# Optimization experiments

Measured on AMD Instinct MI355X. Metric: run time of the kernel, lower is better.

## Reference

```python
import jax, jax.numpy as jnp
import numpy as np

WS = 8   # window size
NH = 8   # num heads


def layernorm(x, g, b, eps=1e-5):
    m = jnp.mean(x, axis=-1, keepdims=True)
    v = jnp.var(x, axis=-1, keepdims=True)
    return (x - m) * jax.lax.rsqrt(v + eps) * g + b


def setup_inputs() -> dict:
    key = jax.random.key(0)
    ks = jax.random.split(key, 8)
    B, C, H, W = 16, 256, 64, 64
    s = 0.02
    inp = {
        "x": jax.random.normal(ks[0], (B, C, H, W), jnp.float32),
        "norm1_g": jnp.ones((C,), jnp.float32),
        "norm1_b": jnp.zeros((C,), jnp.float32),
        "qkv_w": jax.random.normal(ks[1], (3 * C, C), jnp.float32) * s,
        "qkv_b": jnp.zeros((3 * C,), jnp.float32),
        "rel_bias_table": jax.random.normal(ks[2], ((2 * WS - 1) ** 2, NH), jnp.float32) * s,
        "proj_w": jax.random.normal(ks[3], (C, C), jnp.float32) * s,
        "proj_b": jnp.zeros((C,), jnp.float32),
        "norm2_g": jnp.ones((C,), jnp.float32),
        "norm2_b": jnp.zeros((C,), jnp.float32),
        "fc1_w": jax.random.normal(ks[4], (4 * C, C), jnp.float32) * s,
        "fc1_b": jnp.zeros((4 * C,), jnp.float32),
        "fc2_w": jax.random.normal(ks[5], (C, 4 * C), jnp.float32) * s,
        "fc2_b": jnp.zeros((C,), jnp.float32),
    }
    # relative position index (Swin standard), shape (WS*WS, WS*WS), int constant
    coords = np.stack(np.meshgrid(np.arange(WS), np.arange(WS), indexing="ij")).reshape(2, -1)
    rel = (coords[:, :, None] - coords[:, None, :]).transpose(1, 2, 0)
    rel[:, :, 0] += WS - 1
    rel[:, :, 1] += WS - 1
    rel[:, :, 0] *= 2 * WS - 1
    inp["rel_index"] = jnp.asarray(rel.sum(-1), jnp.int32)
    return inp


def reference(x, norm1_g, norm1_b, qkv_w, qkv_b, rel_bias_table, proj_w, proj_b,
              norm2_g, norm2_b, fc1_w, fc1_b, fc2_w, fc2_b, rel_index):
    B, C, H, W = x.shape
    N = WS * WS
    hd = C // NH
    scale = hd ** -0.5

    xs = jnp.transpose(x, (0, 2, 3, 1)).reshape(B, H * W, C)  # b (h w) c
    shortcut = xs

    y = layernorm(xs, norm1_g, norm1_b).reshape(B, H, W, C)
    # window partition -> (B*nW, N, C); shift_size = 0 (default), no cyclic shift / mask
    y = y.reshape(B, H // WS, WS, W // WS, WS, C).transpose(0, 1, 3, 2, 4, 5).reshape(-1, N, C)

    qkv = (y @ qkv_w.T + qkv_b).reshape(-1, N, 3, NH, hd).transpose(2, 0, 3, 1, 4)
    q, k, v = qkv[0], qkv[1], qkv[2]  # each (nW*B, NH, N, hd)

    attn = jnp.einsum("whnd,whmd->whnm", q * scale, k)
    bias = rel_bias_table[rel_index].transpose(2, 0, 1)  # (NH, N, N)
    attn = jax.nn.softmax(attn + bias[None], axis=-1)
    out = jnp.einsum("whnm,whmd->whnd", attn, v).transpose(0, 2, 1, 3).reshape(-1, N, C)
    out = out @ proj_w.T + proj_b

    # window reverse -> (B, H*W, C)
    out = out.reshape(B, H // WS, W // WS, WS, WS, C).transpose(0, 1, 3, 2, 4, 5).reshape(B, H * W, C)

    xs = shortcut + out
    h = layernorm(xs, norm2_g, norm2_b)
    h = jax.nn.gelu(h @ fc1_w.T + fc1_b, approximate=False) @ fc2_w.T + fc2_b
    xs = xs + h

    return jnp.transpose(xs.reshape(B, H, W, C), (0, 3, 1, 2))
```

## Files before the change

### kernel.cpp

```cpp
#include <hip/hip_runtime.h>

typedef unsigned short u16;
typedef __attribute__((ext_vector_type(8))) short short8;
typedef __attribute__((ext_vector_type(4))) float f32x4;

#define MFMA16(a, b, c) __builtin_amdgcn_mfma_f32_16x16x32_bf16((a), (b), (c), 0, 0, 0)
#define WAITV(N) asm volatile("s_waitcnt vmcnt(" #N ")" ::: "memory")
#define BARS() __builtin_amdgcn_s_barrier()
#define MFENCE() asm volatile("" ::: "memory")

__device__ __forceinline__ u16 f2b(float f) {
  unsigned b = __float_as_uint(f);
  b += 0x7FFFu + ((b >> 16) & 1u);
  return (u16)(b >> 16);
}
__device__ __forceinline__ float b2f(u16 u) { return __uint_as_float(((unsigned)u) << 16); }

__device__ __forceinline__ void gload_lds16(const void* g, void* l) {
  __builtin_amdgcn_global_load_lds((const __attribute__((address_space(1))) void*)g,
                                   (__attribute__((address_space(3))) void*)l, 16, 0, 0);
}

__device__ __forceinline__ float fast_gelu(float x) {
  const float u = x * 0.70710678118654752f;
  const float au = fabsf(u);
  float d = 1.f + 0.3275911f * au;
  float tt;
  asm("v_rcp_f32 %0, %1" : "=v"(tt) : "v"(d));
  float p = 1.061405429f * tt - 1.453152027f;
  p = p * tt + 1.421413741f;
  p = p * tt - 0.284496736f;
  p = p * tt + 0.254829592f;
  p = p * tt;
  const float e = __expf(-u * u);
  const float erf_au = 1.f - p * e;
  return 0.5f * x * (1.f + copysignf(erf_au, x));
}

__global__ __launch_bounds__(256) void prep_kernel(
    const float* __restrict__ qkv_w, const float* __restrict__ proj_w,
    const float* __restrict__ fc1_w, const float* __restrict__ fc2_w,
    const float* __restrict__ tbl, const int* __restrict__ ridx,
    u16* __restrict__ wqkv, u16* __restrict__ wproj, u16* __restrict__ wfc1,
    u16* __restrict__ wfc2, float* __restrict__ bfull) {
  int i = blockIdx.x * 256 + threadIdx.x;
  if (i < 196608) {
    wqkv[i] = f2b(qkv_w[i]);
  } else if (i < 262144) {
    wproj[i - 196608] = f2b(proj_w[i - 196608]);
  } else if (i < 524288) {
    wfc1[i - 262144] = f2b(fc1_w[i - 262144]);
  } else if (i < 786432) {
    wfc2[i - 524288] = f2b(fc2_w[i - 524288]);
  } else {
    int j = i - 786432;
    int hm = j >> 12, nm = j & 4095;
    bfull[j] = tbl[ridx[nm] * 8 + hm];
  }
}

__global__ __launch_bounds__(256) void ln1_win_kernel(const float* __restrict__ x,
                                                      const float* __restrict__ g,
                                                      const float* __restrict__ b,
                                                      u16* __restrict__ y,
                                                      u16* __restrict__ xsb) {
  __shared__ float red[2][4][64];
  const int bh = blockIdx.x;
  const int bb = bh >> 6, h = bh & 63;
  const int w = threadIdx.x & 63, cg = threadIdx.x >> 6;
  const float* xp = x + (size_t)bb * 1048576 + (size_t)h * 64 + w;
  float vals[64];
  float s = 0.f, ss = 0.f;
#pragma unroll
  for (int j = 0; j < 64; ++j) {
    float v = xp[(size_t)(cg * 64 + j) * 4096];
    vals[j] = v;
    s += v;
    ss += v * v;
  }
  red[0][cg][w] = s;
  red[1][cg][w] = ss;
  __syncthreads();
  const float S = red[0][0][w] + red[0][1][w] + red[0][2][w] + red[0][3][w];
  const float Q = red[1][0][w] + red[1][1][w] + red[1][2][w] + red[1][3][w];
  const float m = S * (1.f / 256.f);
  const float rstd = rsqrtf(Q * (1.f / 256.f) - m * m + 1e-5f);
  const int win = bb * 64 + ((h >> 3) << 3) + (w >> 3);
  const int tok = ((h & 7) << 3) + (w & 7);
  const size_t base = (size_t)win * 16384 + tok * 256 + cg * 64;
#pragma unroll
  for (int jj = 0; jj < 8; ++jj) {
    short8 o, raw;
#pragma unroll
    for (int q = 0; q < 8; ++q) {
      const int c64 = jj * 8 + q;
      const int c = cg * 64 + c64;
      raw[q] = (short)f2b(vals[c64]);
      o[q] = (short)f2b((vals[c64] - m) * rstd * g[c] + b[c]);
    }
    *(short8*)&y[base + jj * 8] = o;
    *(short8*)&xsb[base + jj * 8] = raw;
  }
}

template <int EPI, int KT, int NNT>
__global__ __launch_bounds__(512, 4) void gemm256(const u16* __restrict__ A,
                                                  const u16* __restrict__ W,
                                                  const float* __restrict__ bias,
                                                  u16* __restrict__ outh,
                                                  float* __restrict__ outf,
                                                  const u16* __restrict__ aux) {
  constexpr int NTK = KT >> 5;
  constexpr int NC = NNT * 128;
  __shared__ __align__(16) u16 As[3][8192];
  __shared__ __align__(16) u16 Bs[3][4096];
  const int xcd = blockIdx.x & 7, ii = blockIdx.x >> 3;
  const int mt = xcd * 32 + ii / NNT;
  const int nt = ii % NNT;
  const int tid = threadIdx.x;
  const int wv = tid >> 6, lane = tid & 63;
  const int wm = wv >> 1, wn = wv & 1;
  const int rowa = tid >> 2;
  const int esl = (((tid & 3) ^ ((tid >> 3) & 3)) << 3);
  const int lr = lane & 15, lg = lane >> 4;
  const int kq = ((lg ^ ((lr >> 1) & 3)) << 3);
  f32x4 acc[4][4];
#pragma unroll
  for (int mi = 0; mi < 4; ++mi)
#pragma unroll
    for (int ni = 0; ni < 4; ++ni) acc[mi][ni] = (f32x4){0.f, 0.f, 0.f, 0.f};
  const u16* Ab = A + (size_t)mt * 256 * KT;
  const u16* Wb = W + (size_t)nt * 128 * KT;

#define STG(BF, T)                                                                      \
  {                                                                                     \
    const int kt_ = (T) << 5;                                                           \
    gload_lds16(Ab + (size_t)rowa * KT + kt_ + esl, &As[BF][tid * 8]);                  \
    gload_lds16(Ab + (size_t)(rowa + 128) * KT + kt_ + esl, &As[BF][tid * 8 + 4096]);   \
    gload_lds16(Wb + (size_t)rowa * KT + kt_ + esl, &Bs[BF][tid * 8]);                  \
  }
#define CMPT(BF)                                                                        \
  {                                                                                     \
    short8 a_[4], b_[4];                                                                \
    _Pragma("unroll") for (int mi = 0; mi < 4; ++mi)                                    \
        a_[mi] = *(const short8*)&As[BF][(wm * 64 + mi * 16 + lr) * 32 + kq];           \
    _Pragma("unroll") for (int ni = 0; ni < 4; ++ni)                                    \
        b_[ni] = *(const short8*)&Bs[BF][(wn * 64 + ni * 16 + lr) * 32 + kq];           \
    _Pragma("unroll") for (int mi = 0; mi < 4; ++mi)                                    \
        _Pragma("unroll") for (int ni = 0; ni < 4; ++ni)                                \
            acc[mi][ni] = MFMA16(a_[mi], b_[ni], acc[mi][ni]);                          \
  }

  STG(0, 0);
  STG(1, 1);
  STG(2, 2);
  int rr = 0;
  for (int t = 0; t < NTK; ++t) {
    if (t + 2 < NTK) {
      WAITV(6);
    } else if (t + 1 < NTK) {
      WAITV(3);
    } else {
      WAITV(0);
    }
    BARS();
    MFENCE();
    CMPT(rr);
    MFENCE();
    BARS();
    if (t + 3 < NTK) STG(rr, t + 3);
    rr = (rr == 2) ? 0 : rr + 1;
  }
#undef STG
#undef CMPT

  const int row0 = mt * 256 + wm * 64 + lg * 4;
  const int col0 = nt * 128 + wn * 64 + lr;

  if constexpr (EPI == 0) {
#pragma unroll
    for (int mi = 0; mi < 4; ++mi)
#pragma unroll
      for (int ni = 0; ni < 4; ++ni) {
        const int col = col0 + ni * 16;
        const int which = col >> 8, cc = col & 255;
        const int head = cc >> 5, hd = cc & 31;
        u16* dst = outh + (size_t)which * 16777216ull;
        const float scl = (which == 0) ? 0.17677669529663689f : 1.0f;
        const float bv = bias[col];
#pragma unroll
        for (int r = 0; r < 4; ++r) {
          const int row = row0 + mi * 16 + r;
          const int win = row >> 6, tk = row & 63;
          dst[(((size_t)(win * 8 + head) << 6) + tk) * 32 + hd] =
              f2b((acc[mi][ni][r] + bv) * scl);
        }
      }
  } else if constexpr (EPI == 2) {
#pragma unroll
    for (int mi = 0; mi < 4; ++mi)
#pragma unroll
      for (int ni = 0; ni < 4; ++ni) {
        const int col = col0 + ni * 16;
        const float bv = bias[col];
#pragma unroll
        for (int r = 0; r < 4; ++r) {
          const int row = row0 + mi * 16 + r;
          outh[(size_t)row * NC + col] = f2b(fast_gelu(acc[mi][ni][r] + bv));
        }
      }
  } else {
#pragma unroll
    for (int mi = 0; mi < 4; ++mi)
#pragma unroll
      for (int ni = 0; ni < 4; ++ni) {
        const int col = col0 + ni * 16;
        const float bv = bias[col];
        const int row = row0 + mi * 16;
        const int win = row >> 6, tk = row & 63;
        const int bb = win >> 6;
        const int h = (((win >> 3) & 7) << 3) + (tk >> 3);
        const int w = ((win & 7) << 3) + (tk & 7);
        f32x4 v;
#pragma unroll
        for (int r = 0; r < 4; ++r)
          v[r] = acc[mi][ni][r] + bv + b2f(aux[(size_t)(row + r) * 256 + col]);
        *(f32x4*)&outf[(((size_t)bb * 256 + col) * 64 + h) * 64 + w] = v;
      }
  }
}

__global__ __launch_bounds__(512, 4) void proj_ln2(const u16* __restrict__ A,
                                                   const u16* __restrict__ W,
                                                   const float* __restrict__ bias,
                                                   const u16* __restrict__ xsb,
                                                   const float* __restrict__ g2,
                                                   const float* __restrict__ b2,
                                                   u16* __restrict__ xs2b,
                                                   u16* __restrict__ h2) {
  __shared__ __align__(16) u16 As[3][4096];
  __shared__ __align__(16) u16 Bs[3][8192];
  __shared__ float redS[4][128], redQ[4][128];
  const int mt = blockIdx.x;
  const int tid = threadIdx.x;
  const int wv = tid >> 6, lane = tid & 63;
  const int wm = wv >> 2, wn = wv & 3;
  const int rowa = tid >> 2;
  const int esl = (((tid & 3) ^ ((tid >> 3) & 3)) << 3);
  const int lr = lane & 15, lg = lane >> 4;
  const int kq = ((lg ^ ((lr >> 1) & 3)) << 3);
  f32x4 acc[4][4];
#pragma unroll
  for (int mi = 0; mi < 4; ++mi)
#pragma unroll
    for (int ni = 0; ni < 4; ++ni) acc[mi][ni] = (f32x4){0.f, 0.f, 0.f, 0.f};
  const u16* Ab = A + (size_t)mt * 128 * 256;

#define STG(BF, T)                                                                      \
  {                                                                                     \
    const int kt_ = (T) << 5;                                                           \
    gload_lds16(Ab + (size_t)rowa * 256 + kt_ + esl, &As[BF][tid * 8]);                 \
    gload_lds16(W + (size_t)rowa * 256 + kt_ + esl, &Bs[BF][tid * 8]);                  \
    gload_lds16(W + (size_t)(rowa + 128) * 256 + kt_ + esl, &Bs[BF][tid * 8 + 4096]);   \
  }
#define CMPT(BF)                                                                        \
  {                                                                                     \
    short8 a_[4], b_[4];                                                                \
    _Pragma("unroll") for (int mi = 0; mi < 4; ++mi)                                    \
        a_[mi] = *(const short8*)&As[BF][(wm * 64 + mi * 16 + lr) * 32 + kq];           \
    _Pragma("unroll") for (int ni = 0; ni < 4; ++ni)                                    \
        b_[ni] = *(const short8*)&Bs[BF][(wn * 64 + ni * 16 + lr) * 32 + kq];           \
    _Pragma("unroll") for (int mi = 0; mi < 4; ++mi)                                    \
        _Pragma("unroll") for (int ni = 0; ni < 4; ++ni)                                \
            acc[mi][ni] = MFMA16(a_[mi], b_[ni], acc[mi][ni]);                          \
  }

  STG(0, 0);
  STG(1, 1);
  STG(2, 2);
  int rr = 0;
  for (int t = 0; t < 8; ++t) {
    if (t + 2 < 8) {
      WAITV(6);
    } else if (t + 1 < 8) {
      WAITV(3);
    } else {
      WAITV(0);
    }
    BARS();
    MFENCE();
    CMPT(rr);
    MFENCE();
    BARS();
    if (t + 3 < 8) STG(rr, t + 3);
    rr = (rr == 2) ? 0 : rr + 1;
  }
#undef STG
#undef CMPT

  const int row0 = mt * 128 + wm * 64 + lg * 4;
  const int col0 = wn * 64 + lr;

#pragma unroll
  for (int mi = 0; mi < 4; ++mi)
#pragma unroll
    for (int ni = 0; ni < 4; ++ni) {
      const int col = col0 + ni * 16;
      const float bv = bias[col];
#pragma unroll
      for (int r = 0; r < 4; ++r)
        acc[mi][ni][r] += bv + b2f(xsb[(size_t)(row0 + mi * 16 + r) * 256 + col]);
    }
#pragma unroll
  for (int mi = 0; mi < 4; ++mi)
#pragma unroll
    for (int r = 0; r < 4; ++r) {
      float s = acc[mi][0][r] + acc[mi][1][r] + acc[mi][2][r] + acc[mi][3][r];
      float q = acc[mi][0][r] * acc[mi][0][r] + acc[mi][1][r] * acc[mi][1][r] +
                acc[mi][2][r] * acc[mi][2][r] + acc[mi][3][r] * acc[mi][3][r];
      s += __shfl_xor(s, 1); q += __shfl_xor(q, 1);
      s += __shfl_xor(s, 2); q += __shfl_xor(q, 2);
      s += __shfl_xor(s, 4); q += __shfl_xor(q, 4);
      s += __shfl_xor(s, 8); q += __shfl_xor(q, 8);
      if (lr == 0) {
        const int rl = wm * 64 + mi * 16 + lg * 4 + r;
        redS[wn][rl] = s;
        redQ[wn][rl] = q;
      }
    }
  __syncthreads();
#pragma unroll
  for (int mi = 0; mi < 4; ++mi)
#pragma unroll
    for (int r = 0; r < 4; ++r) {
      const int rl = wm * 64 + mi * 16 + lg * 4 + r;
      const float S = redS[0][rl] + redS[1][rl] + redS[2][rl] + redS[3][rl];
      const float Q = redQ[0][rl] + redQ[1][rl] + redQ[2][rl] + redQ[3][rl];
      const float m = S * (1.f / 256.f);
      const float rstd = rsqrtf(Q * (1.f / 256.f) - m * m + 1e-5f);
      const size_t row = row0 + mi * 16 + r;
#pragma unroll
      for (int ni = 0; ni < 4; ++ni) {
        const int col = col0 + ni * 16;
        const float v = acc[mi][ni][r];
        xs2b[row * 256 + col] = f2b(v);
        h2[row * 256 + col] = f2b((v - m) * rstd * g2[col] + b2[col]);
      }
    }
}

__global__ __launch_bounds__(64) void attn_kernel(const u16* __restrict__ qkv,
                                                  const float* __restrict__ biasf,
                                                  u16* __restrict__ aout) {
  __shared__ __align__(16) u16 sqk[5120];
  __shared__ __align__(16) u16 vt[2304];
  u16* qs = sqk;
  u16* ks = sqk + 2560;
  u16* pp = sqk;
  const int wh = blockIdx.x;
  const int head = wh & 7;
  const int win = wh >> 3;
  const int lane = threadIdx.x;
  const int lr = lane & 15, lg = lane >> 4;
  const u16* qg = qkv + (size_t)wh * 2048;
  const u16* kg = qkv + 16777216ull + (size_t)wh * 2048;
  const u16* vg = qkv + 33554432ull + (size_t)wh * 2048;
#pragma unroll
  for (int i = 0; i < 4; ++i) {
    int ch = i * 64 + lane;
    int r = ch >> 2, qo = (ch & 3) * 8;
    *(short8*)&qs[r * 40 + qo] = *(const short8*)&qg[r * 32 + qo];
    *(short8*)&ks[r * 40 + qo] = *(const short8*)&kg[r * 32 + qo];
  }
  {
    short8 v0 = *(const short8*)&vg[(size_t)lane * 32];
    short8 v1 = *(const short8*)&vg[(size_t)lane * 32 + 8];
    short8 v2 = *(const short8*)&vg[(size_t)lane * 32 + 16];
    short8 v3 = *(const short8*)&vg[(size_t)lane * 32 + 24];
#pragma unroll
    for (int j = 0; j < 8; ++j) {
      vt[j * 72 + lane] = (u16)v0[j];
      vt[(8 + j) * 72 + lane] = (u16)v1[j];
      vt[(16 + j) * 72 + lane] = (u16)v2[j];
      vt[(24 + j) * 72 + lane] = (u16)v3[j];
    }
  }
  __syncthreads();
  f32x4 sf[4][4];
#pragma unroll
  for (int mi = 0; mi < 4; ++mi)
#pragma unroll
    for (int ni = 0; ni < 4; ++ni) sf[mi][ni] = (f32x4){0.f, 0.f, 0.f, 0.f};
  {
    short8 a[4], bq[4];
#pragma unroll
    for (int mi = 0; mi < 4; ++mi) a[mi] = *(const short8*)&qs[(mi * 16 + lr) * 40 + lg * 8];
#pragma unroll
    for (int ni = 0; ni < 4; ++ni) bq[ni] = *(const short8*)&ks[(ni * 16 + lr) * 40 + lg * 8];
#pragma unroll
    for (int mi = 0; mi < 4; ++mi)
#pragma unroll
      for (int ni = 0; ni < 4; ++ni) sf[mi][ni] = MFMA16(a[mi], bq[ni], sf[mi][ni]);
  }
  __syncthreads();
  const float* bh = biasf + (size_t)head * 4096;
#pragma unroll
  for (int mi = 0; mi < 4; ++mi) {
#pragma unroll
    for (int r = 0; r < 4; ++r) {
      const int n = mi * 16 + lg * 4 + r;
      float v0 = sf[mi][0][r] + bh[n * 64 + lr];
      float v1 = sf[mi][1][r] + bh[n * 64 + 16 + lr];
      float v2 = sf[mi][2][r] + bh[n * 64 + 32 + lr];
      float v3 = sf[mi][3][r] + bh[n * 64 + 48 + lr];
      float mx = fmaxf(fmaxf(v0, v1), fmaxf(v2, v3));
      mx = fmaxf(mx, __shfl_xor(mx, 1));
      mx = fmaxf(mx, __shfl_xor(mx, 2));
      mx = fmaxf(mx, __shfl_xor(mx, 4));
      mx = fmaxf(mx, __shfl_xor(mx, 8));
      float e0 = __expf(v0 - mx), e1 = __expf(v1 - mx);
      float e2 = __expf(v2 - mx), e3 = __expf(v3 - mx);
      float sm = e0 + e1 + e2 + e3;
      sm += __shfl_xor(sm, 1);
      sm += __shfl_xor(sm, 2);
      sm += __shfl_xor(sm, 4);
      sm += __shfl_xor(sm, 8);
      const float inv = 1.f / sm;
      pp[n * 72 + lr] = f2b(e0 * inv);
      pp[n * 72 + 16 + lr] = f2b(e1 * inv);
      pp[n * 72 + 32 + lr] = f2b(e2 * inv);
      pp[n * 72 + 48 + lr] = f2b(e3 * inv);
    }
  }
  __syncthreads();
  f32x4 o[4][2];
#pragma unroll
  for (int mi = 0; mi < 4; ++mi)
#pragma unroll
    for (int ni = 0; ni < 2; ++ni) o[mi][ni] = (f32x4){0.f, 0.f, 0.f, 0.f};
#pragma unroll
  for (int kk = 0; kk < 2; ++kk) {
    short8 pa[4], vb[2];
#pragma unroll
    for (int mi = 0; mi < 4; ++mi)
      pa[mi] = *(const short8*)&pp[(mi * 16 + lr) * 72 + kk * 32 + lg * 8];
#pragma unroll
    for (int ni = 0; ni < 2; ++ni)
      vb[ni] = *(const short8*)&vt[(ni * 16 + lr) * 72 + kk * 32 + lg * 8];
#pragma unroll
    for (int mi = 0; mi < 4; ++mi)
#pragma unroll
      for (int ni = 0; ni < 2; ++ni) o[mi][ni] = MFMA16(pa[mi], vb[ni], o[mi][ni]);
  }
  u16* op = aout + (size_t)win * 16384 + head * 32;
#pragma unroll
  for (int mi = 0; mi < 4; ++mi)
#pragma unroll
    for (int ni = 0; ni < 2; ++ni)
#pragma unroll
      for (int r = 0; r < 4; ++r) {
        const int n = mi * 16 + lg * 4 + r;
        op[(size_t)n * 256 + ni * 16 + lr] = f2b(o[mi][ni][r]);
      }
}

extern "C" void kernel_launch(void* const* d_in, const int* in_sizes, int n_in,
                              void* d_out, int out_size, void* d_ws, size_t ws_size,
                              hipStream_t stream) {
  const float* x = (const float*)d_in[0];
  const float* n1g = (const float*)d_in[1];
  const float* n1b = (const float*)d_in[2];
  const float* qkv_w = (const float*)d_in[3];
  const float* qkv_b = (const float*)d_in[4];
  const float* tbl = (const float*)d_in[5];
  const float* proj_w = (const float*)d_in[6];
  const float* proj_b = (const float*)d_in[7];
  const float* n2g = (const float*)d_in[8];
  const float* n2b = (const float*)d_in[9];
  const float* fc1_w = (const float*)d_in[10];
  const float* fc1_b = (const float*)d_in[11];
  const float* fc2_w = (const float*)d_in[12];
  const float* fc2_b = (const float*)d_in[13];
  const int* relidx = (const int*)d_in[14];
  float* outp = (float*)d_out;

  char* w = (char*)d_ws;
  const size_t Mi = 1ull << 20;
  if (ws_size < 237 * Mi) return;
  u16* Y = (u16*)(w + 0);
  u16* qb = (u16*)(w + 32 * Mi);
  u16* aout = (u16*)(w + 0);
  u16* xs2b = (u16*)(w + 0);
  u16* h2 = (u16*)(w + 32 * Mi);
  u16* xsb = (u16*)(w + 128 * Mi);
  u16* h1 = (u16*)(w + 64 * Mi);
  u16* wqkv = (u16*)(w + 192 * Mi);
  u16* wproj = wqkv + 196608;
  u16* wfc1 = wproj + 65536;
  u16* wfc2 = wfc1 + 262144;
  float* bfull = (float*)(w + 192 * Mi + 1572864);

  prep_kernel<<<3200, 256, 0, stream>>>(qkv_w, proj_w, fc1_w, fc2_w, tbl, relidx, wqkv,
                                        wproj, wfc1, wfc2, bfull);
  ln1_win_kernel<<<1024, 256, 0, stream>>>(x, n1g, n1b, Y, xsb);
  gemm256<0, 256, 6><<<1536, 512, 0, stream>>>(Y, wqkv, qkv_b, qb, nullptr, nullptr);
  attn_kernel<<<8192, 64, 0, stream>>>(qb, bfull, aout);
  proj_ln2<<<512, 512, 0, stream>>>(aout, wproj, proj_b, xsb, n2g, n2b, xs2b, h2);
  gemm256<2, 256, 8><<<2048, 512, 0, stream>>>(h2, wfc1, fc1_b, h1, nullptr, nullptr);
  gemm256<3, 1024, 2><<<512, 512, 0, stream>>>(h1, wfc2, fc2_b, nullptr, outp, xs2b);
}
```

Measured before the change: 348.0 us.

## Shrink GEMM tiles to 128x128 with 256-thread blocks and row-major QKV output

Replaces the 256x128 GEMM tile (512 threads) with a 128x128 tile on 256 threads, doubling the grid and retuning the staging loads and wait counts. The aim is more blocks per CU and better load balance, at the cost of less reuse per loaded tile. It also raises wave priority around the MFMA sequences with s_setprio. The QKV epilogue now writes plain row-major (token, channel) output, and the attention kernel reads with a 256-element stride, replacing the scattered per-head stores with contiguous ones.

```diff
diff --git a/kernel.cpp b/kernel.cpp
--- a/kernel.cpp
+++ b/kernel.cpp
@@ -104,7 +104,7 @@
 }
 
 template <int EPI, int KT, int NNT>
-__global__ __launch_bounds__(512, 4) void gemm256(const u16* __restrict__ A,
+__global__ __launch_bounds__(256, 3) void gemm_bt(const u16* __restrict__ A,
                                                   const u16* __restrict__ W,
                                                   const float* __restrict__ bias,
                                                   u16* __restrict__ outh,
@@ -112,16 +112,17 @@
                                                   const u16* __restrict__ aux) {
   constexpr int NTK = KT >> 5;
   constexpr int NC = NNT * 128;
-  __shared__ __align__(16) u16 As[3][8192];
+  __shared__ __align__(16) u16 As[3][4096];
   __shared__ __align__(16) u16 Bs[3][4096];
   const int xcd = blockIdx.x & 7, ii = blockIdx.x >> 3;
-  const int mt = xcd * 32 + ii / NNT;
+  const int mt = xcd * 64 + ii / NNT;
   const int nt = ii % NNT;
   const int tid = threadIdx.x;
   const int wv = tid >> 6, lane = tid & 63;
-  const int wm = wv >> 1, wn = wv & 1;
-  const int rowa = tid >> 2;
-  const int esl = (((tid & 3) ^ ((tid >> 3) & 3)) << 3);
+  const int wr = (wv >> 1) << 6;
+  const int wc = (wv & 1) << 6;
+  const int lrow4 = lane >> 2;
+  const int srcslot = (((lane & 3) ^ ((lane >> 3) & 3)) << 3);
   const int lr = lane & 15, lg = lane >> 4;
   const int kq = ((lg ^ ((lr >> 1) & 3)) << 3);
   f32x4 acc[4][4];
@@ -129,26 +130,31 @@
   for (int mi = 0; mi < 4; ++mi)
 #pragma unroll
     for (int ni = 0; ni < 4; ++ni) acc[mi][ni] = (f32x4){0.f, 0.f, 0.f, 0.f};
-  const u16* Ab = A + (size_t)mt * 256 * KT;
+  const u16* Ab = A + (size_t)mt * 128 * KT;
   const u16* Wb = W + (size_t)nt * 128 * KT;
 
 #define STG(BF, T)                                                                      \
   {                                                                                     \
     const int kt_ = (T) << 5;                                                           \
-    gload_lds16(Ab + (size_t)rowa * KT + kt_ + esl, &As[BF][tid * 8]);                  \
-    gload_lds16(Ab + (size_t)(rowa + 128) * KT + kt_ + esl, &As[BF][tid * 8 + 4096]);   \
-    gload_lds16(Wb + (size_t)rowa * KT + kt_ + esl, &Bs[BF][tid * 8]);                  \
+    _Pragma("unroll") for (int i_ = 0; i_ < 2; ++i_) {                                  \
+      const int row_ = i_ * 64 + wv * 16 + lrow4;                                       \
+      const int lo_ = i_ * 2048 + wv * 512;                                             \
+      gload_lds16(Ab + (size_t)row_ * KT + kt_ + srcslot, &As[BF][lo_]);                \
+      gload_lds16(Wb + (size_t)row_ * KT + kt_ + srcslot, &Bs[BF][lo_]);                \
+    }                                                                                   \
   }
 #define CMPT(BF)                                                                        \
   {                                                                                     \
     short8 a_[4], b_[4];                                                                \
     _Pragma("unroll") for (int mi = 0; mi < 4; ++mi)                                    \
-        a_[mi] = *(const short8*)&As[BF][(wm * 64 + mi * 16 + lr) * 32 + kq];           \
+        a_[mi] = *(const short8*)&As[BF][(wr + mi * 16 + lr) * 32 + kq];                \
     _Pragma("unroll") for (int ni = 0; ni < 4; ++ni)                                    \
-        b_[ni] = *(const short8*)&Bs[BF][(wn * 64 + ni * 16 + lr) * 32 + kq];           \
+        b_[ni] = *(const short8*)&Bs[BF][(wc + ni * 16 + lr) * 32 + kq];                \
+    __builtin_amdgcn_s_setprio(1);                                                      \
     _Pragma("unroll") for (int mi = 0; mi < 4; ++mi)                                    \
         _Pragma("unroll") for (int ni = 0; ni < 4; ++ni)                                \
             acc[mi][ni] = MFMA16(a_[mi], b_[ni], acc[mi][ni]);                          \
+    __builtin_amdgcn_s_setprio(0);                                                      \
   }
 
   STG(0, 0);
@@ -157,9 +163,9 @@
   int rr = 0;
   for (int t = 0; t < NTK; ++t) {
     if (t + 2 < NTK) {
-      WAITV(6);
+      WAITV(8);
     } else if (t + 1 < NTK) {
-      WAITV(3);
+      WAITV(4);
     } else {
       WAITV(0);
     }
@@ -174,8 +180,8 @@
 #undef STG
 #undef CMPT
 
-  const int row0 = mt * 256 + wm * 64 + lg * 4;
-  const int col0 = nt * 128 + wn * 64 + lr;
+  const int row0 = mt * 128 + wr + lg * 4;
+  const int col0 = nt * 128 + wc + lr;
 
   if constexpr (EPI == 0) {
 #pragma unroll
@@ -184,16 +190,13 @@
       for (int ni = 0; ni < 4; ++ni) {
         const int col = col0 + ni * 16;
         const int which = col >> 8, cc = col & 255;
-        const int head = cc >> 5, hd = cc & 31;
         u16* dst = outh + (size_t)which * 16777216ull;
         const float scl = (which == 0) ? 0.17677669529663689f : 1.0f;
         const float bv = bias[col];
 #pragma unroll
         for (int r = 0; r < 4; ++r) {
           const int row = row0 + mi * 16 + r;
-          const int win = row >> 6, tk = row & 63;
-          dst[(((size_t)(win * 8 + head) << 6) + tk) * 32 + hd] =
-              f2b((acc[mi][ni][r] + bv) * scl);
+          dst[(size_t)row * 256 + cc] = f2b((acc[mi][ni][r] + bv) * scl);
         }
       }
   } else if constexpr (EPI == 2) {
@@ -270,9 +273,11 @@
         a_[mi] = *(const short8*)&As[BF][(wm * 64 + mi * 16 + lr) * 32 + kq];           \
     _Pragma("unroll") for (int ni = 0; ni < 4; ++ni)                                    \
         b_[ni] = *(const short8*)&Bs[BF][(wn * 64 + ni * 16 + lr) * 32 + kq];           \
+    __builtin_amdgcn_s_setprio(1);                                                      \
     _Pragma("unroll") for (int mi = 0; mi < 4; ++mi)                                    \
         _Pragma("unroll") for (int ni = 0; ni < 4; ++ni)                                \
             acc[mi][ni] = MFMA16(a_[mi], b_[ni], acc[mi][ni]);                          \
+    __builtin_amdgcn_s_setprio(0);                                                      \
   }
 
   STG(0, 0);
@@ -362,21 +367,22 @@
   const int win = wh >> 3;
   const int lane = threadIdx.x;
   const int lr = lane & 15, lg = lane >> 4;
-  const u16* qg = qkv + (size_t)wh * 2048;
-  const u16* kg = qkv + 16777216ull + (size_t)wh * 2048;
-  const u16* vg = qkv + 33554432ull + (size_t)wh * 2048;
+  const size_t rbase = (size_t)win * 16384 + head * 32;
+  const u16* qg = qkv + rbase;
+  const u16* kg = qkv + 16777216ull + rbase;
+  const u16* vg = qkv + 33554432ull + rbase;
 #pragma unroll
   for (int i = 0; i < 4; ++i) {
     int ch = i * 64 + lane;
     int r = ch >> 2, qo = (ch & 3) * 8;
-    *(short8*)&qs[r * 40 + qo] = *(const short8*)&qg[r * 32 + qo];
-    *(short8*)&ks[r * 40 + qo] = *(const short8*)&kg[r * 32 + qo];
+    *(short8*)&qs[r * 40 + qo] = *(const short8*)&qg[(size_t)r * 256 + qo];
+    *(short8*)&ks[r * 40 + qo] = *(const short8*)&kg[(size_t)r * 256 + qo];
   }
   {
-    short8 v0 = *(const short8*)&vg[(size_t)lane * 32];
-    short8 v1 = *(const short8*)&vg[(size_t)lane * 32 + 8];
-    short8 v2 = *(const short8*)&vg[(size_t)lane * 32 + 16];
-    short8 v3 = *(const short8*)&vg[(size_t)lane * 32 + 24];
+    short8 v0 = *(const short8*)&vg[(size_t)lane * 256];
+    short8 v1 = *(const short8*)&vg[(size_t)lane * 256 + 8];
+    short8 v2 = *(const short8*)&vg[(size_t)lane * 256 + 16];
+    short8 v3 = *(const short8*)&vg[(size_t)lane * 256 + 24];
 #pragma unroll
     for (int j = 0; j < 8; ++j) {
       vt[j * 72 + lane] = (u16)v0[j];
@@ -503,9 +509,9 @@
   prep_kernel<<<3200, 256, 0, stream>>>(qkv_w, proj_w, fc1_w, fc2_w, tbl, relidx, wqkv,
                                         wproj, wfc1, wfc2, bfull);
   ln1_win_kernel<<<1024, 256, 0, stream>>>(x, n1g, n1b, Y, xsb);
-  gemm256<0, 256, 6><<<1536, 512, 0, stream>>>(Y, wqkv, qkv_b, qb, nullptr, nullptr);
+  gemm_bt<0, 256, 6><<<3072, 256, 0, stream>>>(Y, wqkv, qkv_b, qb, nullptr, nullptr);
   attn_kernel<<<8192, 64, 0, stream>>>(qb, bfull, aout);
   proj_ln2<<<512, 512, 0, stream>>>(aout, wproj, proj_b, xsb, n2g, n2b, xs2b, h2);
-  gemm256<2, 256, 8><<<2048, 512, 0, stream>>>(h2, wfc1, fc1_b, h1, nullptr, nullptr);
-  gemm256<3, 1024, 2><<<512, 512, 0, stream>>>(h1, wfc2, fc2_b, nullptr, outp, xs2b);
-}
+  gemm_bt<2, 256, 8><<<4096, 256, 0, stream>>>(h2, wfc1, fc1_b, h1, nullptr, nullptr);
+  gemm_bt<3, 1024, 2><<<1024, 256, 0, stream>>>(h1, wfc2, fc2_b, nullptr, outp, xs2b);
+}
```

After: 338.7 us. -2.7%, faster.
